# Performance work log

Measured on AMD Instinct MI355X. Metric: run time of the kernel, lower is better.

The kernel has to match this reference:

```python
import jax, jax.numpy as jnp
import numpy as np

D_MODEL = 512
N_HEADS = 8
D_HEAD = D_MODEL // N_HEADS
B = 8
N = 1024
EPS = 1e-5  # torch LayerNorm default


def setup_inputs() -> dict:
    key = jax.random.key(0)
    ks = jax.random.split(key, 12)
    x = jax.random.normal(ks[0], (B, N, D_MODEL), dtype=jnp.float32)
    adj = (jax.random.uniform(ks[1], (B, N, N)) < 0.05).astype(jnp.float32)
    s = 1.0 / np.sqrt(D_MODEL)
    def lin(kw, kb):
        W = jax.random.uniform(kw, (D_MODEL, D_MODEL), minval=-s, maxval=s, dtype=jnp.float32)
        b = jax.random.uniform(kb, (D_MODEL,), minval=-s, maxval=s, dtype=jnp.float32)
        return W, b
    Wq, bq = lin(ks[2], ks[3])
    Wk, bk = lin(ks[4], ks[5])
    Wv, bv = lin(ks[6], ks[7])
    Wo, bo = lin(ks[8], ks[9])
    gamma = jnp.ones((D_MODEL,), dtype=jnp.float32)
    beta = jnp.zeros((D_MODEL,), dtype=jnp.float32)
    return {"x": x, "adj": adj, "Wq": Wq, "bq": bq, "Wk": Wk, "bk": bk,
            "Wv": Wv, "bv": bv, "Wo": Wo, "bo": bo, "gamma": gamma, "beta": beta}


def reference(x, adj, Wq, bq, Wk, bk, Wv, bv, Wo, bo, gamma, beta):
    Bsz, n, _ = x.shape
    # QKV projections -> [b, h, n, d]
    def proj(W, b):
        y = x @ W.T + b
        return y.reshape(Bsz, n, N_HEADS, D_HEAD).transpose(0, 2, 1, 3)
    q, k, v = proj(Wq, bq), proj(Wk, bk), proj(Wv, bv)
    scores = jnp.einsum('bhqd,bhkd->bhqk', q, k) / np.sqrt(D_HEAD)
    # adjacency mask + self-loops, broadcast over heads
    mask = (adj + jnp.eye(n, dtype=adj.dtype)[None]) > 0  # [b, n, n]
    scores = jnp.where(mask[:, None], scores, -jnp.inf)
    attn = jax.nn.softmax(scores, axis=-1)  # dropout is identity in eval
    out = jnp.einsum('bhqk,bhkd->bhqd', attn, v)
    out = out.transpose(0, 2, 1, 3).reshape(Bsz, n, D_MODEL)
    out = out @ Wo.T + bo
    # residual + LayerNorm
    h = x + out
    mu = jnp.mean(h, axis=-1, keepdims=True)
    var = jnp.mean(jnp.square(h - mu), axis=-1, keepdims=True)
    return (h - mu) * jax.lax.rsqrt(var + EPS) * gamma + beta
```

## Files before the change

kernel.cpp:

```cpp
#include <hip/hip_runtime.h>

typedef __bf16 bf16;
typedef bf16 bf16x8 __attribute__((ext_vector_type(8)));
typedef bf16 bf16x4 __attribute__((ext_vector_type(4)));
typedef bf16 bf16x2 __attribute__((ext_vector_type(2)));
typedef float f32x4 __attribute__((ext_vector_type(4)));
typedef unsigned long long u64;
typedef unsigned int u32;

#define B_SZ 8
#define N_SEQ 1024
#define DMODEL 512
#define N_HEADS 8
#define D_HEAD 64
#define M_ROWS 8192

#define QSCALE 0.18033688011112042f

static constexpr size_t OFF_XB   = 0;
static constexpr size_t OFF_WQKV = (size_t)M_ROWS * DMODEL * 2;
static constexpr size_t OFF_WO   = OFF_WQKV + (size_t)1536 * 512 * 2;
static constexpr size_t OFF_BQKV = OFF_WO + (size_t)512 * 512 * 2;
static constexpr size_t OFF_Q    = OFF_BQKV + 1536 * 4;
static constexpr size_t OFF_K    = OFF_Q + (size_t)64 * 1024 * 64 * 2;
static constexpr size_t OFF_V    = OFF_K + (size_t)64 * 1024 * 64 * 2;
static constexpr size_t OFF_MASK = OFF_V + (size_t)64 * 1024 * 64 * 2;

#define PREP_X_BLK 4096
#define PREP_W_BLK 4102
#define PREP_M_BLK 32768

__device__ __forceinline__ f32x4 mfma16(bf16x8 a, bf16x8 b, f32x4 c) {
  return __builtin_amdgcn_mfma_f32_16x16x32_bf16(a, b, c, 0, 0, 0);
}

__device__ __forceinline__ int sidx(int row, int col) {
  return (row << 6) + (col ^ ((row & 7) << 3));
}

__device__ __forceinline__ void gload16(const void* g, void* l) {
  __builtin_amdgcn_global_load_lds(
      (const __attribute__((address_space(1))) void*)g,
      (__attribute__((address_space(3))) void*)l, 16, 0, 0);
}

__global__ void k_prep(const float* __restrict__ x, const float* __restrict__ adj,
                       const float* __restrict__ Wq, const float* __restrict__ Wk,
                       const float* __restrict__ Wv, const float* __restrict__ Wo,
                       const float* __restrict__ bq, const float* __restrict__ bk,
                       const float* __restrict__ bv,
                       bf16* __restrict__ xb, bf16* __restrict__ wqkv,
                       bf16* __restrict__ wo, float* __restrict__ bqkv,
                       u64* __restrict__ maskb) {
  int b = blockIdx.x;
  if (b < PREP_X_BLK) {
    int i = b * 256 + threadIdx.x;
    float4 v = reinterpret_cast<const float4*>(x)[i];
    bf16x4 o = { (bf16)v.x, (bf16)v.y, (bf16)v.z, (bf16)v.w };
    *reinterpret_cast<bf16x4*>(xb + (size_t)i * 4) = o;
  } else if (b < PREP_X_BLK + PREP_W_BLK) {
    int tid = (b - PREP_X_BLK) * 256 + threadIdx.x;
    if (tid < 1536 * 512) {
      int row = tid >> 9;
      const float* Wsrc = row < 512 ? Wq : row < 1024 ? Wk : Wv;
      wqkv[tid] = (bf16)Wsrc[((row & 511) << 9) | (tid & 511)];
    } else if (tid < 1536 * 512 + 512 * 512) {
      int t = tid - 1536 * 512;
      wo[t] = (bf16)Wo[t];
    } else if (tid < 1536 * 512 + 512 * 512 + 1536) {
      int t = tid - (1536 * 512 + 512 * 512);
      bqkv[t] = t < 512 ? bq[t] : t < 1024 ? bk[t - 512] : bv[t - 1024];
    }
  } else {
    int idx = (b - (PREP_X_BLK + PREP_W_BLK)) * 256 + threadIdx.x;
    int q = (idx >> 10) & 1023, k = idx & 1023;
    bool pred = (adj[idx] > 0.f) || (q == k);
    u64 bal = __ballot(pred);
    if ((threadIdx.x & 63) == 0) maskb[idx >> 6] = bal;
  }
}

__global__ __launch_bounds__(256) void k_gemm(const bf16* __restrict__ A,
    const bf16* __restrict__ W, int ncols, int mode,
    const float* __restrict__ bias, const float* __restrict__ xres,
    bf16* __restrict__ oq, bf16* __restrict__ okk, bf16* __restrict__ ov,
    bf16* __restrict__ oh) {
  __shared__ bf16 Al[128 * 64];
  __shared__ bf16 Bl[128 * 64];
  int nbx = ncols >> 7;
  int cpx = gridDim.x >> 3;
  int wid = (blockIdx.x & 7) * cpx + (blockIdx.x >> 3);
  int bx = wid % nbx, by = wid / nbx;
  int m0 = by << 7, n0 = bx << 7;
  int tid = threadIdx.x, lane = tid & 63, w = tid >> 6;
  int wr = (w >> 1) << 6, wc = (w & 1) << 6;
  int lrow = lane & 15, lg = lane >> 4, lko = lg * 8;
  int rl = lane >> 3;
  int csw = ((lane & 7) ^ rl) << 3;

  const bf16* Asrc = A + (size_t)(m0 + w * 32 + rl) * DMODEL + csw;
  const bf16* Wsrc = W + (size_t)(n0 + w * 32 + rl) * DMODEL + csw;
  bf16* Adst = &Al[(w * 4) * 512];
  bf16* Bdst = &Bl[(w * 4) * 512];

  f32x4 acc[4][4];
#pragma unroll
  for (int i = 0; i < 4; i++)
#pragma unroll
    for (int j = 0; j < 4; j++) acc[i][j] = f32x4{0.f, 0.f, 0.f, 0.f};

  for (int k0 = 0; k0 < DMODEL; k0 += 64) {
    __syncthreads();
#pragma unroll
    for (int i = 0; i < 4; i++) {
      gload16(Asrc + k0 + (size_t)i * 8 * DMODEL, Adst + i * 512);
      gload16(Wsrc + k0 + (size_t)i * 8 * DMODEL, Bdst + i * 512);
    }
    __syncthreads();

    bf16x8 afr[4][2], bfr[4][2];
#pragma unroll
    for (int i = 0; i < 4; i++) {
      afr[i][0] = *reinterpret_cast<const bf16x8*>(&Al[sidx(wr + i * 16 + lrow, lko)]);
      afr[i][1] = *reinterpret_cast<const bf16x8*>(&Al[sidx(wr + i * 16 + lrow, 32 + lko)]);
      bfr[i][0] = *reinterpret_cast<const bf16x8*>(&Bl[sidx(wc + i * 16 + lrow, lko)]);
      bfr[i][1] = *reinterpret_cast<const bf16x8*>(&Bl[sidx(wc + i * 16 + lrow, 32 + lko)]);
    }
#pragma unroll
    for (int i = 0; i < 4; i++)
#pragma unroll
      for (int j = 0; j < 4; j++) {
        acc[i][j] = mfma16(afr[i][0], bfr[j][0], acc[i][j]);
        acc[i][j] = mfma16(afr[i][1], bfr[j][1], acc[i][j]);
      }
  }

  int rbase = lg * 4;
  if (mode == 0) {
#pragma unroll
    for (int i = 0; i < 4; i++) {
      int row0 = m0 + wr + i * 16 + rbase;
#pragma unroll
      for (int j = 0; j < 4; j++) {
        int col = n0 + wc + j * 16 + lrow;
        int which = col >> 9, c2 = col & 511, hh = c2 >> 6, dd = c2 & 63;
        float bi = bias[col];
        if (which == 2) {
          int bb = row0 >> 10, nn = row0 & 1023;
          bf16x4 pack;
#pragma unroll
          for (int r = 0; r < 4; r++) pack[r] = (bf16)(acc[i][j][r] + bi);
          *reinterpret_cast<bf16x4*>(
              &ov[(((size_t)bb * N_HEADS + hh) * D_HEAD + dd) * N_SEQ + nn]) = pack;
        } else {
          bf16* dst = which == 0 ? oq : okk;
          float scl = which == 0 ? QSCALE : 1.0f;
#pragma unroll
          for (int r = 0; r < 4; r++) {
            int gm = row0 + r;
            int bb = gm >> 10, nn = gm & 1023;
            dst[(((size_t)bb * N_HEADS + hh) * N_SEQ + nn) * D_HEAD + dd] =
                (bf16)((acc[i][j][r] + bi) * scl);
          }
        }
      }
    }
  } else {
#pragma unroll
    for (int i = 0; i < 4; i++) {
      int row0 = m0 + wr + i * 16 + rbase;
#pragma unroll
      for (int j = 0; j < 4; j++) {
        int col = n0 + wc + j * 16 + lrow;
        float bi = bias[col];
#pragma unroll
        for (int r = 0; r < 4; r++) {
          int gm = row0 + r;
          float y = acc[i][j][r] + bi + xres[(size_t)gm * DMODEL + col];
          oh[(size_t)gm * DMODEL + col] = (bf16)y;
        }
      }
    }
  }
}

__global__ __launch_bounds__(256, 4) void k_attn(const bf16* __restrict__ Qb,
    const bf16* __restrict__ Kb, const bf16* __restrict__ Vtg,
    const u64* __restrict__ maskb, bf16* __restrict__ attn_out) {
  __shared__ bf16 Kl[2][64 * 64];
  __shared__ bf16 Vt[2][64 * 64];

  int bid = blockIdx.x;
  int work = ((bid & 7) << 7) | (bid >> 3);
  int bh = work >> 4, qb = work & 15;
  int bb = bh >> 3, hh = bh & 7;
  int tid = threadIdx.x, lane = tid & 63, w = tid >> 6;
  int lrow = lane & 15, lg = lane >> 4;
  int rl = lane >> 3;
  int csw = ((lane & 7) ^ rl) << 3;
  int q0w = qb * 64 + w * 16;

  const bf16* Qh = Qb + (size_t)bh * N_SEQ * D_HEAD;
  const bf16* Kh = Kb + (size_t)bh * N_SEQ * D_HEAD;
  const bf16* Vh = Vtg + (size_t)bh * D_HEAD * N_SEQ;
  const u32* m32 = (const u32*)(maskb + (size_t)bb * N_SEQ * 16);

  const bf16* Ksrc = Kh + (size_t)(w * 16 + rl) * D_HEAD + csw;
  const bf16* Vsrc = Vh + (size_t)(w * 16 + rl) * N_SEQ + csw;

  bf16x8 qf0 = *reinterpret_cast<const bf16x8*>(&Qh[(q0w + lrow) * 64 + lg * 8]);
  bf16x8 qf1 = *reinterpret_cast<const bf16x8*>(&Qh[(q0w + lrow) * 64 + 32 + lg * 8]);

  f32x4 o[4];
#pragma unroll
  for (int d = 0; d < 4; d++) o[d] = f32x4{0.f, 0.f, 0.f, 0.f};
  float ls = 0.f;

#define STAGE(buf, kt0)                                                     \
  {                                                                         \
    _Pragma("unroll") for (int i = 0; i < 2; i++) {                         \
      gload16(Ksrc + (size_t)(kt0) * 64 + i * 512, &Kl[buf][(w * 2 + i) * 512]); \
      gload16(Vsrc + (size_t)i * 8192 + (kt0), &Vt[buf][(w * 2 + i) * 512]);     \
    }                                                                       \
  }

  STAGE(0, 0);

  for (int kt = 0; kt < 16; kt++) {
    int cur = kt & 1;
    int kt0 = kt << 6;
    int midx = ((q0w + lrow) * 16 + kt) * 2;
    u32 mlo = m32[midx], mhi = m32[midx + 1];

    if (kt < 15) STAGE(cur ^ 1, kt0 + 64);

    __builtin_amdgcn_sched_barrier(0);
    if (kt < 15) { asm volatile("s_waitcnt vmcnt(6)" ::: "memory"); }
    else         { asm volatile("s_waitcnt vmcnt(2)" ::: "memory"); }
    __builtin_amdgcn_sched_barrier(0);
    __builtin_amdgcn_s_barrier();
    __builtin_amdgcn_sched_barrier(0);

    f32x4 sc[4];
#pragma unroll
    for (int t = 0; t < 4; t++) {
      bf16x8 kf0 = *reinterpret_cast<const bf16x8*>(&Kl[cur][sidx(t * 16 + lrow, lg * 8)]);
      bf16x8 kf1 = *reinterpret_cast<const bf16x8*>(&Kl[cur][sidx(t * 16 + lrow, 32 + lg * 8)]);
      sc[t] = f32x4{0.f, 0.f, 0.f, 0.f};
      __builtin_amdgcn_s_setprio(1);
      sc[t] = mfma16(kf0, qf0, sc[t]);
      sc[t] = mfma16(kf1, qf1, sc[t]);
      __builtin_amdgcn_s_setprio(0);
    }

    bf16x8 pa[2];
#pragma unroll
    for (int m = 0; m < 2; m++) {
      u32 mw = m == 0 ? mlo : mhi;
#pragma unroll
      for (int j = 0; j < 8; j++) {
        int sh = ((j >> 2) << 4) + lg * 4 + (j & 3);
        int t = 2 * m + (j >> 2), r = j & 3;
        bool bit = (mw >> sh) & 1u;
        float pv = bit ? exp2f(sc[t][r]) : 0.f;
        ls += pv;
        pa[m][j] = (bf16)pv;
      }
    }

#pragma unroll
    for (int d = 0; d < 4; d++) {
#pragma unroll
      for (int m = 0; m < 2; m++) {
        bf16x4 va = *reinterpret_cast<const bf16x4*>(
            &Vt[cur][sidx(d * 16 + lrow, m * 32 + lg * 4)]);
        bf16x4 vb = *reinterpret_cast<const bf16x4*>(
            &Vt[cur][sidx(d * 16 + lrow, m * 32 + 16 + lg * 4)]);
        bf16x8 vf = {va[0], va[1], va[2], va[3], vb[0], vb[1], vb[2], vb[3]};
        __builtin_amdgcn_s_setprio(1);
        o[d] = mfma16(vf, pa[m], o[d]);
        __builtin_amdgcn_s_setprio(0);
      }
    }

    __builtin_amdgcn_sched_barrier(0);
    asm volatile("s_waitcnt lgkmcnt(0)" ::: "memory");
    __builtin_amdgcn_s_barrier();
    __builtin_amdgcn_sched_barrier(0);
  }

  ls += __shfl_xor(ls, 16);
  ls += __shfl_xor(ls, 32);
  float inv = 1.f / ls;

  int gq = q0w + lrow;
#pragma unroll
  for (int d = 0; d < 4; d++) {
    bf16x4 pk;
#pragma unroll
    for (int r = 0; r < 4; r++) pk[r] = (bf16)(o[d][r] * inv);
    *reinterpret_cast<bf16x4*>(
        &attn_out[((size_t)(bb * N_SEQ + gq)) * DMODEL + hh * 64 + d * 16 + lg * 4]) = pk;
  }
#undef STAGE
}

__global__ __launch_bounds__(256) void k_ln(const bf16* __restrict__ hb,
    const float* __restrict__ gamma, const float* __restrict__ beta,
    float* __restrict__ out) {
  int row = blockIdx.x, tid = threadIdx.x;
  bf16x2 v2 = *reinterpret_cast<const bf16x2*>(hb + (size_t)row * DMODEL + tid * 2);
  float vx = (float)v2[0], vy = (float)v2[1];
  float s = vx + vy, ss = vx * vx + vy * vy;
#pragma unroll
  for (int off = 1; off < 64; off <<= 1) {
    s += __shfl_xor(s, off);
    ss += __shfl_xor(ss, off);
  }
  __shared__ float as_[4], ass_[4];
  int w = tid >> 6;
  if ((tid & 63) == 0) { as_[w] = s; ass_[w] = ss; }
  __syncthreads();
  s = as_[0] + as_[1] + as_[2] + as_[3];
  ss = ass_[0] + ass_[1] + ass_[2] + ass_[3];
  float mu = s * (1.f / 512.f);
  float var = ss * (1.f / 512.f) - mu * mu;
  float rstd = rsqrtf(var + 1e-5f);
  float2 g = reinterpret_cast<const float2*>(gamma)[tid];
  float2 bt = reinterpret_cast<const float2*>(beta)[tid];
  float2 o;
  o.x = (vx - mu) * rstd * g.x + bt.x;
  o.y = (vy - mu) * rstd * g.y + bt.y;
  reinterpret_cast<float2*>(out + (size_t)row * DMODEL)[tid] = o;
}

extern "C" void kernel_launch(void* const* d_in, const int* in_sizes, int n_in,
                              void* d_out, int out_size, void* d_ws, size_t ws_size,
                              hipStream_t stream) {
  const float* x     = (const float*)d_in[0];
  const float* adj   = (const float*)d_in[1];
  const float* Wq    = (const float*)d_in[2];
  const float* bq    = (const float*)d_in[3];
  const float* Wk    = (const float*)d_in[4];
  const float* bk    = (const float*)d_in[5];
  const float* Wv    = (const float*)d_in[6];
  const float* bv    = (const float*)d_in[7];
  const float* Wo    = (const float*)d_in[8];
  const float* bo    = (const float*)d_in[9];
  const float* gamma = (const float*)d_in[10];
  const float* beta  = (const float*)d_in[11];

  char* ws = (char*)d_ws;
  bf16* xb    = (bf16*)(ws + OFF_XB);
  bf16* wqkv  = (bf16*)(ws + OFF_WQKV);
  bf16* wo    = (bf16*)(ws + OFF_WO);
  float* bqkv = (float*)(ws + OFF_BQKV);
  bf16* Qb    = (bf16*)(ws + OFF_Q);
  bf16* Kb    = (bf16*)(ws + OFF_K);
  bf16* Vb    = (bf16*)(ws + OFF_V);
  u64* maskb  = (u64*)(ws + OFF_MASK);
  bf16* attn  = xb;
  bf16* hb    = (bf16*)(ws + OFF_Q);
  float* out  = (float*)d_out;

  k_prep<<<dim3(PREP_X_BLK + PREP_W_BLK + PREP_M_BLK), dim3(256), 0, stream>>>(
      x, adj, Wq, Wk, Wv, Wo, bq, bk, bv, xb, wqkv, wo, bqkv, maskb);

  k_gemm<<<dim3((M_ROWS / 128) * (1536 / 128)), dim3(256), 0, stream>>>(
      xb, wqkv, 1536, 0, bqkv, nullptr, Qb, Kb, Vb, nullptr);

  k_attn<<<dim3(1024), dim3(256), 0, stream>>>(Qb, Kb, Vb, maskb, attn);

  k_gemm<<<dim3((M_ROWS / 128) * (512 / 128)), dim3(256), 0, stream>>>(
      attn, wo, 512, 1, bo, x, nullptr, nullptr, nullptr, hb);

  k_ln<<<dim3(M_ROWS), dim3(256), 0, stream>>>(hb, gamma, beta, out);
}
```

Baseline: 106.0 us.

## Overlap adjacency mask packing and Wo conversion with QKV GEMM launch

Moves the adjacency bitmask packing and Wo bf16 conversion out of the prep kernel and into extra blocks of a dedicated QKV GEMM kernel, so the memory-bound mask work (reading the 32MB adj) runs concurrently with the compute-bound GEMM blocks. The GEMM kernel is specialized (no mode branch), and the output-projection GEMM loses its unused QKV epilogue. Risk: GEMM blocks are dispatched first then 33k light blocks share CUs with them, possibly contending for bandwidth.

```diff
diff --git a/kernel.cpp b/kernel.cpp
--- a/kernel.cpp
+++ b/kernel.cpp
@@ -27,8 +27,11 @@
 static constexpr size_t OFF_MASK = OFF_V + (size_t)64 * 1024 * 64 * 2;
 
 #define PREP_X_BLK 4096
-#define PREP_W_BLK 4102
-#define PREP_M_BLK 32768
+#define PREP_W_BLK 3078
+
+#define G1_GEMM 768
+#define G1_MASK 32768
+#define G1_WO   1024
 
 __device__ __forceinline__ f32x4 mfma16(bf16x8 a, bf16x8 b, f32x4 c) {
   return __builtin_amdgcn_mfma_f32_16x16x32_bf16(a, b, c, 0, 0, 0);
@@ -44,46 +47,136 @@
       (__attribute__((address_space(3))) void*)l, 16, 0, 0);
 }
 
-__global__ void k_prep(const float* __restrict__ x, const float* __restrict__ adj,
+__global__ void k_prep(const float* __restrict__ x,
                        const float* __restrict__ Wq, const float* __restrict__ Wk,
-                       const float* __restrict__ Wv, const float* __restrict__ Wo,
+                       const float* __restrict__ Wv,
                        const float* __restrict__ bq, const float* __restrict__ bk,
                        const float* __restrict__ bv,
                        bf16* __restrict__ xb, bf16* __restrict__ wqkv,
-                       bf16* __restrict__ wo, float* __restrict__ bqkv,
-                       u64* __restrict__ maskb) {
+                       float* __restrict__ bqkv) {
   int b = blockIdx.x;
   if (b < PREP_X_BLK) {
     int i = b * 256 + threadIdx.x;
     float4 v = reinterpret_cast<const float4*>(x)[i];
     bf16x4 o = { (bf16)v.x, (bf16)v.y, (bf16)v.z, (bf16)v.w };
     *reinterpret_cast<bf16x4*>(xb + (size_t)i * 4) = o;
-  } else if (b < PREP_X_BLK + PREP_W_BLK) {
+  } else {
     int tid = (b - PREP_X_BLK) * 256 + threadIdx.x;
     if (tid < 1536 * 512) {
       int row = tid >> 9;
       const float* Wsrc = row < 512 ? Wq : row < 1024 ? Wk : Wv;
       wqkv[tid] = (bf16)Wsrc[((row & 511) << 9) | (tid & 511)];
-    } else if (tid < 1536 * 512 + 512 * 512) {
+    } else if (tid < 1536 * 512 + 1536) {
       int t = tid - 1536 * 512;
-      wo[t] = (bf16)Wo[t];
-    } else if (tid < 1536 * 512 + 512 * 512 + 1536) {
-      int t = tid - (1536 * 512 + 512 * 512);
       bqkv[t] = t < 512 ? bq[t] : t < 1024 ? bk[t - 512] : bv[t - 1024];
     }
-  } else {
-    int idx = (b - (PREP_X_BLK + PREP_W_BLK)) * 256 + threadIdx.x;
+  }
+}
+
+__global__ __launch_bounds__(256) void k_gemm1f(const bf16* __restrict__ A,
+    const bf16* __restrict__ W, const float* __restrict__ bias,
+    bf16* __restrict__ oq, bf16* __restrict__ okk, bf16* __restrict__ ov,
+    const float* __restrict__ adj, const float* __restrict__ Wo,
+    bf16* __restrict__ wo, u64* __restrict__ maskb) {
+  __shared__ bf16 Al[128 * 64];
+  __shared__ bf16 Bl[128 * 64];
+  int bid = blockIdx.x;
+
+  if (bid >= G1_GEMM + G1_MASK) {
+    int t = (bid - G1_GEMM - G1_MASK) * 256 + threadIdx.x;
+    wo[t] = (bf16)Wo[t];
+    return;
+  }
+  if (bid >= G1_GEMM) {
+    int idx = (bid - G1_GEMM) * 256 + threadIdx.x;
     int q = (idx >> 10) & 1023, k = idx & 1023;
     bool pred = (adj[idx] > 0.f) || (q == k);
     u64 bal = __ballot(pred);
     if ((threadIdx.x & 63) == 0) maskb[idx >> 6] = bal;
+    return;
+  }
+
+  const int nbx = 12;
+  int wid = (bid & 7) * (G1_GEMM / 8) + (bid >> 3);
+  int bx = wid % nbx, by = wid / nbx;
+  int m0 = by << 7, n0 = bx << 7;
+  int tid = threadIdx.x, lane = tid & 63, w = tid >> 6;
+  int wr = (w >> 1) << 6, wc = (w & 1) << 6;
+  int lrow = lane & 15, lg = lane >> 4, lko = lg * 8;
+  int rl = lane >> 3;
+  int csw = ((lane & 7) ^ rl) << 3;
+
+  const bf16* Asrc = A + (size_t)(m0 + w * 32 + rl) * DMODEL + csw;
+  const bf16* Wsrc = W + (size_t)(n0 + w * 32 + rl) * DMODEL + csw;
+  bf16* Adst = &Al[(w * 4) * 512];
+  bf16* Bdst = &Bl[(w * 4) * 512];
+
+  f32x4 acc[4][4];
+#pragma unroll
+  for (int i = 0; i < 4; i++)
+#pragma unroll
+    for (int j = 0; j < 4; j++) acc[i][j] = f32x4{0.f, 0.f, 0.f, 0.f};
+
+  for (int k0 = 0; k0 < DMODEL; k0 += 64) {
+    __syncthreads();
+#pragma unroll
+    for (int i = 0; i < 4; i++) {
+      gload16(Asrc + k0 + (size_t)i * 8 * DMODEL, Adst + i * 512);
+      gload16(Wsrc + k0 + (size_t)i * 8 * DMODEL, Bdst + i * 512);
+    }
+    __syncthreads();
+
+    bf16x8 afr[4][2], bfr[4][2];
+#pragma unroll
+    for (int i = 0; i < 4; i++) {
+      afr[i][0] = *reinterpret_cast<const bf16x8*>(&Al[sidx(wr + i * 16 + lrow, lko)]);
+      afr[i][1] = *reinterpret_cast<const bf16x8*>(&Al[sidx(wr + i * 16 + lrow, 32 + lko)]);
+      bfr[i][0] = *reinterpret_cast<const bf16x8*>(&Bl[sidx(wc + i * 16 + lrow, lko)]);
+      bfr[i][1] = *reinterpret_cast<const bf16x8*>(&Bl[sidx(wc + i * 16 + lrow, 32 + lko)]);
+    }
+#pragma unroll
+    for (int i = 0; i < 4; i++)
+#pragma unroll
+      for (int j = 0; j < 4; j++) {
+        acc[i][j] = mfma16(afr[i][0], bfr[j][0], acc[i][j]);
+        acc[i][j] = mfma16(afr[i][1], bfr[j][1], acc[i][j]);
+      }
+  }
+
+  int rbase = lg * 4;
+#pragma unroll
+  for (int i = 0; i < 4; i++) {
+    int row0 = m0 + wr + i * 16 + rbase;
+#pragma unroll
+    for (int j = 0; j < 4; j++) {
+      int col = n0 + wc + j * 16 + lrow;
+      int which = col >> 9, c2 = col & 511, hh = c2 >> 6, dd = c2 & 63;
+      float bi = bias[col];
+      if (which == 2) {
+        int bb = row0 >> 10, nn = row0 & 1023;
+        bf16x4 pack;
+#pragma unroll
+        for (int r = 0; r < 4; r++) pack[r] = (bf16)(acc[i][j][r] + bi);
+        *reinterpret_cast<bf16x4*>(
+            &ov[(((size_t)bb * N_HEADS + hh) * D_HEAD + dd) * N_SEQ + nn]) = pack;
+      } else {
+        bf16* dst = which == 0 ? oq : okk;
+        float scl = which == 0 ? QSCALE : 1.0f;
+#pragma unroll
+        for (int r = 0; r < 4; r++) {
+          int gm = row0 + r;
+          int bb = gm >> 10, nn = gm & 1023;
+          dst[(((size_t)bb * N_HEADS + hh) * N_SEQ + nn) * D_HEAD + dd] =
+              (bf16)((acc[i][j][r] + bi) * scl);
+        }
+      }
+    }
   }
 }
 
 __global__ __launch_bounds__(256) void k_gemm(const bf16* __restrict__ A,
-    const bf16* __restrict__ W, int ncols, int mode,
+    const bf16* __restrict__ W, int ncols,
     const float* __restrict__ bias, const float* __restrict__ xres,
-    bf16* __restrict__ oq, bf16* __restrict__ okk, bf16* __restrict__ ov,
     bf16* __restrict__ oh) {
   __shared__ bf16 Al[128 * 64];
   __shared__ bf16 Bl[128 * 64];
@@ -136,49 +229,18 @@
   }
 
   int rbase = lg * 4;
-  if (mode == 0) {
-#pragma unroll
-    for (int i = 0; i < 4; i++) {
-      int row0 = m0 + wr + i * 16 + rbase;
-#pragma unroll
-      for (int j = 0; j < 4; j++) {
-        int col = n0 + wc + j * 16 + lrow;
-        int which = col >> 9, c2 = col & 511, hh = c2 >> 6, dd = c2 & 63;
-        float bi = bias[col];
-        if (which == 2) {
-          int bb = row0 >> 10, nn = row0 & 1023;
-          bf16x4 pack;
-#pragma unroll
-          for (int r = 0; r < 4; r++) pack[r] = (bf16)(acc[i][j][r] + bi);
-          *reinterpret_cast<bf16x4*>(
-              &ov[(((size_t)bb * N_HEADS + hh) * D_HEAD + dd) * N_SEQ + nn]) = pack;
-        } else {
-          bf16* dst = which == 0 ? oq : okk;
-          float scl = which == 0 ? QSCALE : 1.0f;
-#pragma unroll
-          for (int r = 0; r < 4; r++) {
-            int gm = row0 + r;
-            int bb = gm >> 10, nn = gm & 1023;
-            dst[(((size_t)bb * N_HEADS + hh) * N_SEQ + nn) * D_HEAD + dd] =
-                (bf16)((acc[i][j][r] + bi) * scl);
-          }
-        }
-      }
-    }
-  } else {
-#pragma unroll
-    for (int i = 0; i < 4; i++) {
-      int row0 = m0 + wr + i * 16 + rbase;
-#pragma unroll
-      for (int j = 0; j < 4; j++) {
-        int col = n0 + wc + j * 16 + lrow;
-        float bi = bias[col];
-#pragma unroll
-        for (int r = 0; r < 4; r++) {
-          int gm = row0 + r;
-          float y = acc[i][j][r] + bi + xres[(size_t)gm * DMODEL + col];
-          oh[(size_t)gm * DMODEL + col] = (bf16)y;
-        }
+#pragma unroll
+  for (int i = 0; i < 4; i++) {
+    int row0 = m0 + wr + i * 16 + rbase;
+#pragma unroll
+    for (int j = 0; j < 4; j++) {
+      int col = n0 + wc + j * 16 + lrow;
+      float bi = bias[col];
+#pragma unroll
+      for (int r = 0; r < 4; r++) {
+        int gm = row0 + r;
+        float y = acc[i][j][r] + bi + xres[(size_t)gm * DMODEL + col];
+        oh[(size_t)gm * DMODEL + col] = (bf16)y;
       }
     }
   }
@@ -363,16 +425,16 @@
   bf16* hb    = (bf16*)(ws + OFF_Q);
   float* out  = (float*)d_out;
 
-  k_prep<<<dim3(PREP_X_BLK + PREP_W_BLK + PREP_M_BLK), dim3(256), 0, stream>>>(
-      x, adj, Wq, Wk, Wv, Wo, bq, bk, bv, xb, wqkv, wo, bqkv, maskb);
-
-  k_gemm<<<dim3((M_ROWS / 128) * (1536 / 128)), dim3(256), 0, stream>>>(
-      xb, wqkv, 1536, 0, bqkv, nullptr, Qb, Kb, Vb, nullptr);
+  k_prep<<<dim3(PREP_X_BLK + PREP_W_BLK), dim3(256), 0, stream>>>(
+      x, Wq, Wk, Wv, bq, bk, bv, xb, wqkv, bqkv);
+
+  k_gemm1f<<<dim3(G1_GEMM + G1_MASK + G1_WO), dim3(256), 0, stream>>>(
+      xb, wqkv, bqkv, Qb, Kb, Vb, adj, Wo, wo, maskb);
 
   k_attn<<<dim3(1024), dim3(256), 0, stream>>>(Qb, Kb, Vb, maskb, attn);
 
   k_gemm<<<dim3((M_ROWS / 128) * (512 / 128)), dim3(256), 0, stream>>>(
-      attn, wo, 512, 1, bo, x, nullptr, nullptr, nullptr, hb);
+      attn, wo, 512, bo, x, hb);
 
   k_ln<<<dim3(M_ROWS), dim3(256), 0, stream>>>(hb, gamma, beta, out);
 }
```

After: 123.5 us. +16.5%, slower.
